# Kernel optimization log

Measured on AMD Instinct MI355X. Metric: run time of the kernel, lower is better.

The kernel has to match this reference:

```python
import jax, jax.numpy as jnp
import numpy as np

B, L, J, D_MODEL, N_HIDDEN = 8, 2048, 2048, 1024, 1024


def setup_inputs() -> dict:
    key = jax.random.key(0)
    ks = jax.random.split(key, 6)
    scale = 1.0 / np.sqrt(D_MODEL)
    return {
        "q": jax.random.normal(ks[0], (B, L, D_MODEL), dtype=jnp.float32),
        "k": jax.random.normal(ks[1], (B, J, D_MODEL), dtype=jnp.float32),
        "v": jax.random.normal(ks[2], (B, J, D_MODEL), dtype=jnp.float32),
        "mask": jnp.zeros((B, L, J), dtype=jnp.float32),
        # Linear(d_model, n_hidden, bias=False) weights, stored [n_hidden, d_model] like torch
        "W_q": jax.random.normal(ks[3], (N_HIDDEN, D_MODEL), dtype=jnp.float32) * scale,
        "W_k": jax.random.normal(ks[4], (N_HIDDEN, D_MODEL), dtype=jnp.float32) * scale,
        "W_v": jax.random.normal(ks[5], (N_HIDDEN, D_MODEL), dtype=jnp.float32) * scale,
    }


def reference(q, k, v, mask, W_q, W_k, W_v):
    # Linear projections (torch Linear: x @ W.T)
    qp = jnp.einsum('bld,hd->blh', q, W_q)
    kp = jnp.einsum('bjd,hd->bjh', k, W_k)
    vp = jnp.einsum('bjd,hd->bjh', v, W_v)
    # scaled dot-product scores [B, L, J]
    scores = jnp.einsum('blh,bjh->blj', qp, kp) / jnp.sqrt(jnp.float32(N_HIDDEN)).astype(qp.dtype)
    scores = scores + mask
    attn = jax.nn.softmax(scores, axis=-1)
    return jnp.einsum('blj,bjh->blh', attn, vp)
```

## Files before the change

kernel.cpp:

```cpp
#include <hip/hip_runtime.h>
#include <hip/hip_fp16.h>

typedef _Float16 f16;
typedef __attribute__((ext_vector_type(8))) _Float16 f16x8;
typedef __attribute__((ext_vector_type(4))) _Float16 f16x4;
typedef __attribute__((ext_vector_type(4))) float f32x4;

#define BM 128
#define BN 128
#define BK 64

__device__ __forceinline__ void gll16(const void* src, void* dst) {
  __builtin_amdgcn_global_load_lds((const __attribute__((address_space(1))) void*)src,
                                   (__attribute__((address_space(3))) void*)dst,
                                   16, 0, 0);
}

template<int MODE>
__global__ __launch_bounds__(256, 3)
void gemm_bt(const f16* __restrict__ Aall, const f16* __restrict__ Ball,
             void* __restrict__ Call,
             int M, int N, int K, int lda, int ldb, int ldc,
             long strideA, long strideB, long strideC,
             const float* __restrict__ maskAll, long strideMask,
             float* __restrict__ lvec, float scale)
{
  __shared__ __align__(16) f16 smbuf[BM * BK + BN * BK];
  f16* smA = smbuf;
  f16* smB = smbuf + BM * BK;

  unsigned gx = gridDim.x, gy = gridDim.y;
  unsigned id = (blockIdx.z * gy + blockIdx.y) * gx + blockIdx.x;
  unsigned nwg = gx * gy * gridDim.z;
  unsigned swz = (id & 7) * (nwg >> 3) + (id >> 3);
  unsigned bx = swz % gx, rem = swz / gx;
  unsigned by = rem % gy, bz = rem / gy;

  const int z = bz;
  const f16* A = Aall + (long)z * strideA;
  const f16* B = Ball + (long)z * strideB;

  const int tid  = threadIdx.x;
  const int wid  = tid >> 6;
  const int lane = tid & 63;
  const int wm = wid >> 1;
  const int wn = wid & 1;
  const int lr = lane & 15;
  const int g  = lane >> 4;

  const long brow = (long)by * BM;
  const long bcol = (long)bx * BN;
  const int  nt   = K / BK;

  f32x4 acc[4][4] = {};

  auto stA = [&](int t) {
    #pragma unroll
    for (int i = 0; i < 4; ++i) {
      int c  = i * 256 + tid;
      int r  = c >> 3;
      int sl = (c & 7) ^ (r & 7);
      gll16(A + (brow + r) * (long)lda + t * BK + sl * 8, &smA[c * 8]);
    }
  };
  auto stB = [&](int t) {
    #pragma unroll
    for (int i = 0; i < 4; ++i) {
      int c  = i * 256 + tid;
      int r  = c >> 3;
      int sl = (c & 7) ^ (r & 7);
      gll16(B + (bcol + r) * (long)ldb + t * BK + sl * 8, &smB[c * 8]);
    }
  };

  for (int t = 0; t < nt; ++t) {
    stA(t); stB(t);
    __syncthreads();
    f16x8 af[8], bf[8];
    #pragma unroll
    for (int fm = 0; fm < 4; ++fm)
      #pragma unroll
      for (int ks = 0; ks < 2; ++ks) {
        int r = wm * 64 + fm * 16 + lr;
        af[fm * 2 + ks] = *(const f16x8*)(smA + r * BK + ((ks * 4 + g) ^ (r & 7)) * 8);
      }
    #pragma unroll
    for (int fn = 0; fn < 4; ++fn)
      #pragma unroll
      for (int ks = 0; ks < 2; ++ks) {
        int r = wn * 64 + fn * 16 + lr;
        bf[fn * 2 + ks] = *(const f16x8*)(smB + r * BK + ((ks * 4 + g) ^ (r & 7)) * 8);
      }
    #pragma unroll
    for (int fm = 0; fm < 4; ++fm)
      #pragma unroll
      for (int fn = 0; fn < 4; ++fn)
        #pragma unroll
        for (int ks = 0; ks < 2; ++ks)
          acc[fm][fn] = __builtin_amdgcn_mfma_f32_16x16x32_f16(
              af[fm * 2 + ks], bf[fn * 2 + ks], acc[fm][fn], 0, 0, 0);
    __syncthreads();
  }

  const int rb = (lane >> 4) * 4;

  if (MODE == 0) {
    f16* C = (f16*)Call + (long)z * strideC;
    #pragma unroll
    for (int m = 0; m < 4; ++m)
      #pragma unroll
      for (int j = 0; j < 4; ++j) {
        long grow = brow + wm * 64 + m * 16 + rb + j;
        #pragma unroll
        for (int n = 0; n < 4; ++n) {
          long gcol = bcol + wn * 64 + n * 16 + lr;
          C[grow * ldc + gcol] = (f16)acc[m][n][j];
        }
      }
  } else if (MODE == 1) {
    f16* smM = smbuf;
    const float* mask = maskAll + (long)z * strideMask;
    #pragma unroll
    for (int i = 0; i < 8; ++i) {
      int e = i * 2048 + tid * 8;
      int r = e >> 7, c = e & 127;
      const float* s = mask + (brow + r) * (long)ldc + bcol + c;
      float4 lo = *(const float4*)s, hi = *(const float4*)(s + 4);
      f16x8 o;
      o[0] = (f16)lo.x; o[1] = (f16)lo.y; o[2] = (f16)lo.z; o[3] = (f16)lo.w;
      o[4] = (f16)hi.x; o[5] = (f16)hi.y; o[6] = (f16)hi.z; o[7] = (f16)hi.w;
      *(f16x8*)(smM + r * 128 + (c ^ ((r & 7) << 3))) = o;
    }
    __syncthreads();
    #pragma unroll
    for (int m = 0; m < 4; ++m)
      #pragma unroll
      for (int j = 0; j < 4; ++j) {
        int lrow = wm * 64 + m * 16 + rb + j;
        float s = 0.f;
        #pragma unroll
        for (int n = 0; n < 4; ++n) {
          int lcol = wn * 64 + n * 16 + lr;
          int a = lrow * 128 + (lcol ^ ((lrow & 7) << 3));
          float p = __expf(acc[m][n][j] * scale + (float)smM[a]);
          smM[a] = (f16)p;
          s += p;
        }
        s += __shfl_xor(s, 1);
        s += __shfl_xor(s, 2);
        s += __shfl_xor(s, 4);
        s += __shfl_xor(s, 8);
        if (lr == 0)
          lvec[((long)z * M + brow + lrow) * 32 + bx * 2 + wn] = s;
      }
    __syncthreads();
    f16* C = (f16*)Call + (long)z * strideC;
    #pragma unroll
    for (int i = 0; i < 8; ++i) {
      int e = i * 2048 + tid * 8;
      int r = e >> 7, c = e & 127;
      f16x8 o = *(const f16x8*)(smM + r * 128 + (c ^ ((r & 7) << 3)));
      *(f16x8*)(C + (brow + r) * (long)ldc + bcol + c) = o;
    }
  } else {
    float* smO = (float*)smbuf;
    float* C = (float*)Call + (long)z * strideC;
    #pragma unroll
    for (int h = 0; h < 2; ++h) {
      if (wm == h) {
        #pragma unroll
        for (int m = 0; m < 4; ++m)
          #pragma unroll
          for (int j = 0; j < 4; ++j) {
            int lrh = m * 16 + rb + j;
            float inv = 1.0f / lvec[(long)z * M + brow + h * 64 + lrh];
            #pragma unroll
            for (int n = 0; n < 4; ++n) {
              int lcol = wn * 64 + n * 16 + lr;
              smO[lrh * 128 + (lcol ^ ((lrh & 7) << 2))] = acc[m][n][j] * inv;
            }
          }
      }
      __syncthreads();
      #pragma unroll
      for (int i = 0; i < 8; ++i) {
        int e = i * 1024 + tid * 4;
        int r = e >> 7, c = e & 127;
        float4 o = *(const float4*)(smO + r * 128 + (c ^ ((r & 7) << 2)));
        *(float4*)(C + (brow + h * 64 + r) * (long)ldc + bcol + c) = o;
      }
      if (h == 0) __syncthreads();
    }
  }
}

__global__ void cvt_all(const float* __restrict__ q, const float* __restrict__ k,
                        const float* __restrict__ v, const float* __restrict__ Wv,
                        f16* __restrict__ qf, f16* __restrict__ kf, f16* __restrict__ vf,
                        f16* __restrict__ Wvf)
{
  const long NQ4 = 4194304, NW4 = 262144;
  const long total = 3 * NQ4 + NW4;
  for (long i = (long)blockIdx.x * blockDim.x + threadIdx.x; i < total;
       i += (long)gridDim.x * blockDim.x) {
    const float* src; f16* dst; long j = i;
    if      (j <     NQ4) { src = q;  dst = qf; }
    else if (j < 2 * NQ4) { src = k;  dst = kf;  j -= NQ4; }
    else if (j < 3 * NQ4) { src = v;  dst = vf;  j -= 2 * NQ4; }
    else                  { src = Wv; dst = Wvf; j -= 3 * NQ4; }
    float4 vv = ((const float4*)src)[j];
    f16x4 o;
    o[0] = (f16)vv.x; o[1] = (f16)vv.y; o[2] = (f16)vv.z; o[3] = (f16)vv.w;
    ((f16x4*)dst)[j] = o;
  }
}

__global__ void transW(const float* __restrict__ Wq, const float* __restrict__ Wk,
                       f16* __restrict__ WqT, f16* __restrict__ WkT)
{
  __shared__ f16 t[64][65];
  const float* W  = blockIdx.z ? Wk : Wq;
  f16*         WT = blockIdx.z ? WkT : WqT;
  const int h0 = blockIdx.y * 64, d0 = blockIdx.x * 64;
  const int tx = threadIdx.x & 15, ty = threadIdx.x >> 4;
  #pragma unroll
  for (int p = 0; p < 4; ++p) {
    int h = ty + p * 16;
    float4 vv = *(const float4*)(W + (long)(h0 + h) * 1024 + d0 + tx * 4);
    t[tx * 4 + 0][h] = (f16)vv.x;
    t[tx * 4 + 1][h] = (f16)vv.y;
    t[tx * 4 + 2][h] = (f16)vv.z;
    t[tx * 4 + 3][h] = (f16)vv.w;
  }
  __syncthreads();
  #pragma unroll
  for (int p = 0; p < 4; ++p) {
    int d = ty + p * 16;
    f16x4 o;
    o[0] = t[d][tx * 4 + 0];
    o[1] = t[d][tx * 4 + 1];
    o[2] = t[d][tx * 4 + 2];
    o[3] = t[d][tx * 4 + 3];
    *(f16x4*)(WT + (long)(d0 + d) * 1024 + h0 + tx * 4) = o;
  }
}

__global__ void reduce_l(const float* __restrict__ lpart, float* __restrict__ lsum, int n) {
  int i = blockIdx.x * blockDim.x + threadIdx.x;
  if (i < n) {
    float s = 0.f;
    #pragma unroll
    for (int j = 0; j < 32; ++j) s += lpart[(long)i * 32 + j];
    lsum[i] = s;
  }
}

extern "C" void kernel_launch(void* const* d_in, const int* in_sizes, int n_in,
                              void* d_out, int out_size, void* d_ws, size_t ws_size,
                              hipStream_t stream)
{
  const float* q    = (const float*)d_in[0];
  const float* k    = (const float*)d_in[1];
  const float* v    = (const float*)d_in[2];
  const float* mask = (const float*)d_in[3];
  const float* Wq   = (const float*)d_in[4];
  const float* Wk   = (const float*)d_in[5];
  const float* Wv   = (const float*)d_in[6];
  float* out = (float*)d_out;
  char*  ws  = (char*)d_ws;

  f16*   qf    = (f16*)(ws + 0);
  f16*   vf    = (f16*)(ws + 33554432);
  f16*   Pm    = (f16*)(ws + 0);
  f16*   kf    = (f16*)(ws + 67108864);
  f16*   Wvf   = (f16*)(ws + 100663296);
  f16*   WqT   = (f16*)(ws + 102760448);
  f16*   WkT   = (f16*)(ws + 104857600);
  f16*   Gt    = (f16*)(ws + 106954752);
  f16*   qg    = (f16*)(ws + 109051904);
  f16*   vpT   = (f16*)(ws + 142606336);
  float* lpart = (float*)(ws + 176160768);
  float* lsum  = (float*)(ws + 178257920);

  const long L = 2048, J = 2048, D = 1024, H = 1024;

  cvt_all<<<dim3(2048), dim3(256), 0, stream>>>(q, k, v, Wv, qf, kf, vf, Wvf);
  transW<<<dim3(16, 16, 2), dim3(256), 0, stream>>>(Wq, Wk, WqT, WkT);

  gemm_bt<0><<<dim3(1024 / BN, 1024 / BM, 1), dim3(256), 0, stream>>>(
      WkT, WqT, Gt, 1024, 1024, 1024, 1024, 1024, 1024,
      0, 0, 0, nullptr, 0, nullptr, 0.f);

  gemm_bt<0><<<dim3(1024 / BN, 16384 / BM, 1), dim3(256), 0, stream>>>(
      qf, Gt, qg, 16384, 1024, 1024, 1024, 1024, 1024,
      0, 0, 0, nullptr, 0, nullptr, 0.f);

  gemm_bt<0><<<dim3(2048 / BN, 1024 / BM, 8), dim3(256), 0, stream>>>(
      Wvf, vf, vpT, 1024, 2048, 1024, 1024, 1024, 2048,
      0, J * D, H * J, nullptr, 0, nullptr, 0.f);

  gemm_bt<1><<<dim3(2048 / BN, 2048 / BM, 8), dim3(256), 0, stream>>>(
      qg, kf, Pm, 2048, 2048, 1024, 1024, 1024, 2048,
      L * D, J * D, L * J, mask, L * J, lpart, 0.03125f);

  reduce_l<<<dim3(16384 / 256), dim3(256), 0, stream>>>(lpart, lsum, 16384);

  gemm_bt<2><<<dim3(1024 / BN, 2048 / BM, 8), dim3(256), 0, stream>>>(
      Pm, vpT, out, 2048, 1024, 2048, 2048, 2048, 1024,
      L * J, H * J, L * H, nullptr, 0, lsum, 0.f);
}
```

Baseline: 332.6 us.

## Merge launches: fuse conversion kernels, batch independent GEMMs, fold row-sum reduction

```diff
diff --git a/kernel.cpp b/kernel.cpp
--- a/kernel.cpp
+++ b/kernel.cpp
@@ -16,29 +16,30 @@
                                    16, 0, 0);
 }
 
+struct GArgs {
+  const f16* A; const f16* B; void* C;
+  int M, N, K, lda, ldb, ldc;
+  long sA, sB, sC;
+  const float* mask; long sMask;
+  float* lpart; float scale;
+  unsigned gx, gy, gz;
+};
+
 template<int MODE>
-__global__ __launch_bounds__(256, 3)
-void gemm_bt(const f16* __restrict__ Aall, const f16* __restrict__ Ball,
-             void* __restrict__ Call,
-             int M, int N, int K, int lda, int ldb, int ldc,
-             long strideA, long strideB, long strideC,
-             const float* __restrict__ maskAll, long strideMask,
-             float* __restrict__ lvec, float scale)
-{
-  __shared__ __align__(16) f16 smbuf[BM * BK + BN * BK];
+__device__ __forceinline__ void gemm_body(const GArgs ga, unsigned fid,
+                                          f16* smbuf, float* smL)
+{
   f16* smA = smbuf;
   f16* smB = smbuf + BM * BK;
 
-  unsigned gx = gridDim.x, gy = gridDim.y;
-  unsigned id = (blockIdx.z * gy + blockIdx.y) * gx + blockIdx.x;
-  unsigned nwg = gx * gy * gridDim.z;
-  unsigned swz = (id & 7) * (nwg >> 3) + (id >> 3);
-  unsigned bx = swz % gx, rem = swz / gx;
-  unsigned by = rem % gy, bz = rem / gy;
+  unsigned nwg = ga.gx * ga.gy * ga.gz;
+  unsigned swz = (fid & 7) * (nwg >> 3) + (fid >> 3);
+  unsigned bx = swz % ga.gx, rem = swz / ga.gx;
+  unsigned by = rem % ga.gy, bz = rem / ga.gy;
 
   const int z = bz;
-  const f16* A = Aall + (long)z * strideA;
-  const f16* B = Ball + (long)z * strideB;
+  const f16* A = ga.A + (long)z * ga.sA;
+  const f16* B = ga.B + (long)z * ga.sB;
 
   const int tid  = threadIdx.x;
   const int wid  = tid >> 6;
@@ -50,7 +51,17 @@
 
   const long brow = (long)by * BM;
   const long bcol = (long)bx * BN;
-  const int  nt   = K / BK;
+  const int  nt   = ga.K / BK;
+
+  if (MODE == 2) {
+    if (tid < 128) {
+      const float* lp = ga.lpart + ((long)z * ga.M + brow + tid) * 32;
+      float s = 0.f;
+      #pragma unroll
+      for (int j = 0; j < 32; ++j) s += lp[j];
+      smL[tid] = 1.0f / s;
+    }
+  }
 
   f32x4 acc[4][4] = {};
 
@@ -60,7 +71,7 @@
       int c  = i * 256 + tid;
       int r  = c >> 3;
       int sl = (c & 7) ^ (r & 7);
-      gll16(A + (brow + r) * (long)lda + t * BK + sl * 8, &smA[c * 8]);
+      gll16(A + (brow + r) * (long)ga.lda + t * BK + sl * 8, &smA[c * 8]);
     }
   };
   auto stB = [&](int t) {
@@ -69,7 +80,7 @@
       int c  = i * 256 + tid;
       int r  = c >> 3;
       int sl = (c & 7) ^ (r & 7);
-      gll16(B + (bcol + r) * (long)ldb + t * BK + sl * 8, &smB[c * 8]);
+      gll16(B + (bcol + r) * (long)ga.ldb + t * BK + sl * 8, &smB[c * 8]);
     }
   };
 
@@ -105,7 +116,7 @@
   const int rb = (lane >> 4) * 4;
 
   if (MODE == 0) {
-    f16* C = (f16*)Call + (long)z * strideC;
+    f16* C = (f16*)ga.C + (long)z * ga.sC;
     #pragma unroll
     for (int m = 0; m < 4; ++m)
       #pragma unroll
@@ -114,17 +125,17 @@
         #pragma unroll
         for (int n = 0; n < 4; ++n) {
           long gcol = bcol + wn * 64 + n * 16 + lr;
-          C[grow * ldc + gcol] = (f16)acc[m][n][j];
+          C[grow * ga.ldc + gcol] = (f16)acc[m][n][j];
         }
       }
   } else if (MODE == 1) {
     f16* smM = smbuf;
-    const float* mask = maskAll + (long)z * strideMask;
+    const float* mask = ga.mask + (long)z * ga.sMask;
     #pragma unroll
     for (int i = 0; i < 8; ++i) {
       int e = i * 2048 + tid * 8;
       int r = e >> 7, c = e & 127;
-      const float* s = mask + (brow + r) * (long)ldc + bcol + c;
+      const float* s = mask + (brow + r) * (long)ga.ldc + bcol + c;
       float4 lo = *(const float4*)s, hi = *(const float4*)(s + 4);
       f16x8 o;
       o[0] = (f16)lo.x; o[1] = (f16)lo.y; o[2] = (f16)lo.z; o[3] = (f16)lo.w;
@@ -142,7 +153,7 @@
         for (int n = 0; n < 4; ++n) {
           int lcol = wn * 64 + n * 16 + lr;
           int a = lrow * 128 + (lcol ^ ((lrow & 7) << 3));
-          float p = __expf(acc[m][n][j] * scale + (float)smM[a]);
+          float p = __expf(acc[m][n][j] * ga.scale + (float)smM[a]);
           smM[a] = (f16)p;
           s += p;
         }
@@ -151,20 +162,20 @@
         s += __shfl_xor(s, 4);
         s += __shfl_xor(s, 8);
         if (lr == 0)
-          lvec[((long)z * M + brow + lrow) * 32 + bx * 2 + wn] = s;
-      }
-    __syncthreads();
-    f16* C = (f16*)Call + (long)z * strideC;
+          ga.lpart[((long)z * ga.M + brow + lrow) * 32 + bx * 2 + wn] = s;
+      }
+    __syncthreads();
+    f16* C = (f16*)ga.C + (long)z * ga.sC;
     #pragma unroll
     for (int i = 0; i < 8; ++i) {
       int e = i * 2048 + tid * 8;
       int r = e >> 7, c = e & 127;
       f16x8 o = *(const f16x8*)(smM + r * 128 + (c ^ ((r & 7) << 3)));
-      *(f16x8*)(C + (brow + r) * (long)ldc + bcol + c) = o;
+      *(f16x8*)(C + (brow + r) * (long)ga.ldc + bcol + c) = o;
     }
   } else {
     float* smO = (float*)smbuf;
-    float* C = (float*)Call + (long)z * strideC;
+    float* C = (float*)ga.C + (long)z * ga.sC;
     #pragma unroll
     for (int h = 0; h < 2; ++h) {
       if (wm == h) {
@@ -173,7 +184,7 @@
           #pragma unroll
           for (int j = 0; j < 4; ++j) {
             int lrh = m * 16 + rb + j;
-            float inv = 1.0f / lvec[(long)z * M + brow + h * 64 + lrh];
+            float inv = smL[h * 64 + lrh];
             #pragma unroll
             for (int n = 0; n < 4; ++n) {
               int lcol = wn * 64 + n * 16 + lr;
@@ -187,71 +198,79 @@
         int e = i * 1024 + tid * 4;
         int r = e >> 7, c = e & 127;
         float4 o = *(const float4*)(smO + r * 128 + (c ^ ((r & 7) << 2)));
-        *(float4*)(C + (brow + h * 64 + r) * (long)ldc + bcol + c) = o;
+        *(float4*)(C + (brow + h * 64 + r) * (long)ga.ldc + bcol + c) = o;
       }
       if (h == 0) __syncthreads();
     }
   }
 }
 
-__global__ void cvt_all(const float* __restrict__ q, const float* __restrict__ k,
-                        const float* __restrict__ v, const float* __restrict__ Wv,
-                        f16* __restrict__ qf, f16* __restrict__ kf, f16* __restrict__ vf,
-                        f16* __restrict__ Wvf)
-{
-  const long NQ4 = 4194304, NW4 = 262144;
-  const long total = 3 * NQ4 + NW4;
-  for (long i = (long)blockIdx.x * blockDim.x + threadIdx.x; i < total;
-       i += (long)gridDim.x * blockDim.x) {
-    const float* src; f16* dst; long j = i;
-    if      (j <     NQ4) { src = q;  dst = qf; }
-    else if (j < 2 * NQ4) { src = k;  dst = kf;  j -= NQ4; }
-    else if (j < 3 * NQ4) { src = v;  dst = vf;  j -= 2 * NQ4; }
-    else                  { src = Wv; dst = Wvf; j -= 3 * NQ4; }
-    float4 vv = ((const float4*)src)[j];
-    f16x4 o;
-    o[0] = (f16)vv.x; o[1] = (f16)vv.y; o[2] = (f16)vv.z; o[3] = (f16)vv.w;
-    ((f16x4*)dst)[j] = o;
-  }
-}
-
-__global__ void transW(const float* __restrict__ Wq, const float* __restrict__ Wk,
-                       f16* __restrict__ WqT, f16* __restrict__ WkT)
+template<int MODE>
+__global__ __launch_bounds__(256, 3)
+void gemm_single(GArgs ga)
+{
+  __shared__ __align__(16) f16 smbuf[BM * BK + BN * BK];
+  __shared__ float smL[128];
+  gemm_body<MODE>(ga, blockIdx.x, smbuf, smL);
+}
+
+__global__ __launch_bounds__(256, 3)
+void gemm_dual0(GArgs a0, GArgs a1, unsigned n0)
+{
+  __shared__ __align__(16) f16 smbuf[BM * BK + BN * BK];
+  unsigned fid = blockIdx.x;
+  if (fid < n0) gemm_body<0>(a0, fid, smbuf, nullptr);
+  else          gemm_body<0>(a1, fid - n0, smbuf, nullptr);
+}
+
+__global__ void cvt_trans(const float* __restrict__ q, const float* __restrict__ k,
+                          const float* __restrict__ v, const float* __restrict__ Wq,
+                          const float* __restrict__ Wk, const float* __restrict__ Wv,
+                          f16* __restrict__ qf, f16* __restrict__ kf, f16* __restrict__ vf,
+                          f16* __restrict__ Wvf, f16* __restrict__ WqT, f16* __restrict__ WkT)
 {
   __shared__ f16 t[64][65];
-  const float* W  = blockIdx.z ? Wk : Wq;
-  f16*         WT = blockIdx.z ? WkT : WqT;
-  const int h0 = blockIdx.y * 64, d0 = blockIdx.x * 64;
-  const int tx = threadIdx.x & 15, ty = threadIdx.x >> 4;
-  #pragma unroll
-  for (int p = 0; p < 4; ++p) {
-    int h = ty + p * 16;
-    float4 vv = *(const float4*)(W + (long)(h0 + h) * 1024 + d0 + tx * 4);
-    t[tx * 4 + 0][h] = (f16)vv.x;
-    t[tx * 4 + 1][h] = (f16)vv.y;
-    t[tx * 4 + 2][h] = (f16)vv.z;
-    t[tx * 4 + 3][h] = (f16)vv.w;
-  }
-  __syncthreads();
-  #pragma unroll
-  for (int p = 0; p < 4; ++p) {
-    int d = ty + p * 16;
-    f16x4 o;
-    o[0] = t[d][tx * 4 + 0];
-    o[1] = t[d][tx * 4 + 1];
-    o[2] = t[d][tx * 4 + 2];
-    o[3] = t[d][tx * 4 + 3];
-    *(f16x4*)(WT + (long)(d0 + d) * 1024 + h0 + tx * 4) = o;
-  }
-}
-
-__global__ void reduce_l(const float* __restrict__ lpart, float* __restrict__ lsum, int n) {
-  int i = blockIdx.x * blockDim.x + threadIdx.x;
-  if (i < n) {
-    float s = 0.f;
-    #pragma unroll
-    for (int j = 0; j < 32; ++j) s += lpart[(long)i * 32 + j];
-    lsum[i] = s;
+  const unsigned bid = blockIdx.x;
+  if (bid < 512) {
+    const float* W  = (bid & 256) ? Wk : Wq;
+    f16*         WT = (bid & 256) ? WkT : WqT;
+    const int h0 = ((bid >> 4) & 15) * 64, d0 = (bid & 15) * 64;
+    const int tx = threadIdx.x & 15, ty = threadIdx.x >> 4;
+    #pragma unroll
+    for (int p = 0; p < 4; ++p) {
+      int h = ty + p * 16;
+      float4 vv = *(const float4*)(W + (long)(h0 + h) * 1024 + d0 + tx * 4);
+      t[tx * 4 + 0][h] = (f16)vv.x;
+      t[tx * 4 + 1][h] = (f16)vv.y;
+      t[tx * 4 + 2][h] = (f16)vv.z;
+      t[tx * 4 + 3][h] = (f16)vv.w;
+    }
+    __syncthreads();
+    #pragma unroll
+    for (int p = 0; p < 4; ++p) {
+      int d = ty + p * 16;
+      f16x4 o;
+      o[0] = t[d][tx * 4 + 0];
+      o[1] = t[d][tx * 4 + 1];
+      o[2] = t[d][tx * 4 + 2];
+      o[3] = t[d][tx * 4 + 3];
+      *(f16x4*)(WT + (long)(d0 + d) * 1024 + h0 + tx * 4) = o;
+    }
+  } else {
+    const long NQ4 = 4194304, NW4 = 262144;
+    const long total = 3 * NQ4 + NW4;
+    const long nb = 2048;
+    for (long i = (long)(bid - 512) * 256 + threadIdx.x; i < total; i += nb * 256) {
+      const float* src; f16* dst; long j = i;
+      if      (j <     NQ4) { src = q;  dst = qf; }
+      else if (j < 2 * NQ4) { src = k;  dst = kf;  j -= NQ4; }
+      else if (j < 3 * NQ4) { src = v;  dst = vf;  j -= 2 * NQ4; }
+      else                  { src = Wv; dst = Wvf; j -= 3 * NQ4; }
+      float4 vv = ((const float4*)src)[j];
+      f16x4 o;
+      o[0] = (f16)vv.x; o[1] = (f16)vv.y; o[2] = (f16)vv.z; o[3] = (f16)vv.w;
+      ((f16x4*)dst)[j] = o;
+    }
   }
 }
 
@@ -280,32 +299,28 @@
   f16*   qg    = (f16*)(ws + 109051904);
   f16*   vpT   = (f16*)(ws + 142606336);
   float* lpart = (float*)(ws + 176160768);
-  float* lsum  = (float*)(ws + 178257920);
-
-  const long L = 2048, J = 2048, D = 1024, H = 1024;
-
-  cvt_all<<<dim3(2048), dim3(256), 0, stream>>>(q, k, v, Wv, qf, kf, vf, Wvf);
-  transW<<<dim3(16, 16, 2), dim3(256), 0, stream>>>(Wq, Wk, WqT, WkT);
-
-  gemm_bt<0><<<dim3(1024 / BN, 1024 / BM, 1), dim3(256), 0, stream>>>(
-      WkT, WqT, Gt, 1024, 1024, 1024, 1024, 1024, 1024,
-      0, 0, 0, nullptr, 0, nullptr, 0.f);
-
-  gemm_bt<0><<<dim3(1024 / BN, 16384 / BM, 1), dim3(256), 0, stream>>>(
-      qf, Gt, qg, 16384, 1024, 1024, 1024, 1024, 1024,
-      0, 0, 0, nullptr, 0, nullptr, 0.f);
-
-  gemm_bt<0><<<dim3(2048 / BN, 1024 / BM, 8), dim3(256), 0, stream>>>(
-      Wvf, vf, vpT, 1024, 2048, 1024, 1024, 1024, 2048,
-      0, J * D, H * J, nullptr, 0, nullptr, 0.f);
-
-  gemm_bt<1><<<dim3(2048 / BN, 2048 / BM, 8), dim3(256), 0, stream>>>(
-      qg, kf, Pm, 2048, 2048, 1024, 1024, 1024, 2048,
-      L * D, J * D, L * J, mask, L * J, lpart, 0.03125f);
-
-  reduce_l<<<dim3(16384 / 256), dim3(256), 0, stream>>>(lpart, lsum, 16384);
-
-  gemm_bt<2><<<dim3(1024 / BN, 2048 / BM, 8), dim3(256), 0, stream>>>(
-      Pm, vpT, out, 2048, 1024, 2048, 2048, 2048, 1024,
-      L * J, H * J, L * H, nullptr, 0, lsum, 0.f);
-}
+
+  cvt_trans<<<dim3(2560), dim3(256), 0, stream>>>(
+      q, k, v, Wq, Wk, Wv, qf, kf, vf, Wvf, WqT, WkT);
+
+  GArgs aGt = { WkT, WqT, Gt, 1024, 1024, 1024, 1024, 1024, 1024,
+                0, 0, 0, nullptr, 0, nullptr, 0.f, 8, 8, 1 };
+  gemm_single<0><<<dim3(64), dim3(256), 0, stream>>>(aGt);
+
+  GArgs aQg  = { qf, Gt, qg, 16384, 1024, 1024, 1024, 1024, 1024,
+                 0, 0, 0, nullptr, 0, nullptr, 0.f, 8, 128, 1 };
+  GArgs aVpT = { Wvf, vf, vpT, 1024, 2048, 1024, 1024, 1024, 2048,
+                 0, (long)2048 * 1024, (long)1024 * 2048, nullptr, 0, nullptr, 0.f,
+                 16, 8, 8 };
+  gemm_dual0<<<dim3(2048), dim3(256), 0, stream>>>(aQg, aVpT, 1024);
+
+  GArgs aSc = { qg, kf, Pm, 2048, 2048, 1024, 1024, 1024, 2048,
+                (long)2048 * 1024, (long)2048 * 1024, (long)2048 * 2048,
+                mask, (long)2048 * 2048, lpart, 0.03125f, 16, 16, 8 };
+  gemm_single<1><<<dim3(2048), dim3(256), 0, stream>>>(aSc);
+
+  GArgs aPV = { Pm, vpT, out, 2048, 1024, 2048, 2048, 2048, 1024,
+                (long)2048 * 2048, (long)1024 * 2048, (long)2048 * 1024,
+                nullptr, 0, lpart, 0.f, 8, 16, 8 };
+  gemm_single<2><<<dim3(1024), dim3(256), 0, stream>>>(aPV);
+}
```

Measured after the change: 330.6 us. About the same (-0.6%).
